# Kernel tuning notes

Hardware: AMD Instinct MI355X
Metric: run time of the kernel (lower is better)

The kernel has to match this reference:

```python
import jax, jax.numpy as jnp
import numpy as np
import math

D_MODEL = 1024
NHEAD = 16
D_HEAD = D_MODEL // NHEAD
TAU = 300.0
DELTA = 5.0 * 60.0  # delta_minutes -> seconds


def setup_inputs() -> dict:
    key = jax.random.key(0)
    ks = jax.random.split(key, 10)
    B, M = 4, 2048
    H = jax.random.normal(ks[0], (B, M, D_MODEL), dtype=jnp.float32)
    patch_mask = jax.random.randint(ks[1], (B, M), 0, 2).astype(jnp.int32)
    s = 1.0 / math.sqrt(D_MODEL)
    Wq = jax.random.normal(ks[2], (D_MODEL, D_MODEL), dtype=jnp.float32) * s
    bq = jnp.zeros((D_MODEL,), dtype=jnp.float32)
    Wk = jax.random.normal(ks[3], (D_MODEL, D_MODEL), dtype=jnp.float32) * s
    bk = jnp.zeros((D_MODEL,), dtype=jnp.float32)
    Wv = jax.random.normal(ks[4], (D_MODEL, D_MODEL), dtype=jnp.float32) * s
    bv = jnp.zeros((D_MODEL,), dtype=jnp.float32)
    Wo = jax.random.normal(ks[5], (D_MODEL, D_MODEL), dtype=jnp.float32) * s
    bo = jnp.zeros((D_MODEL,), dtype=jnp.float32)
    return {"H": H, "patch_mask": patch_mask, "Wq": Wq, "bq": bq,
            "Wk": Wk, "bk": bk, "Wv": Wv, "bv": bv, "Wo": Wo, "bo": bo}


def _time_bias(M):
    idx = jnp.arange(M)
    dist = jnp.abs(idx[:, None] - idx[None, :]).astype(jnp.float32) * DELTA
    w = jnp.exp(-dist / max(TAU, 1e-6))
    return jnp.log(w + 1e-12)  # (M, M)


def reference(H, patch_mask, Wq, bq, Wk, bk, Wv, bv, Wo, bo):
    B, M, D = H.shape
    nh, dh = NHEAD, D_HEAD
    # projections -> (B, nh, M, dh)
    q = (H @ Wq.T + bq).reshape(B, M, nh, dh).transpose(0, 2, 1, 3)
    k = (H @ Wk.T + bk).reshape(B, M, nh, dh).transpose(0, 2, 1, 3)
    v = (H @ Wv.T + bv).reshape(B, M, nh, dh).transpose(0, 2, 1, 3)
    attn = jnp.einsum('bhqd,bhkd->bhqk', q, k) / math.sqrt(dh)
    attn = attn + _time_bias(M)[None, None, :, :]
    key_pad = patch_mask <= 0  # (B, M)
    attn = jnp.where(key_pad[:, None, None, :], -1e9, attn)
    A = jax.nn.softmax(attn, axis=-1)
    out = jnp.einsum('bhqk,bhkd->bhqd', A, v)
    out = out.transpose(0, 2, 1, 3).reshape(B, M, D)
    out = out @ Wo.T + bo
    out = out * patch_mask[:, :, None].astype(out.dtype)
    return out
```

## Files before the change

### kernel.cpp

```cpp
#include <hip/hip_runtime.h>
#include <stdint.h>

typedef short short8 __attribute__((ext_vector_type(8)));
typedef float f32x4 __attribute__((ext_vector_type(4)));

#define B_    4
#define M_    2048
#define D_    1024
#define NH_   16
#define DH_   64
#define LOG2E 1.44269504f

#if __has_builtin(__builtin_amdgcn_exp2f)
#define EXP2F(x) __builtin_amdgcn_exp2f(x)
#else
#define EXP2F(x) exp2f(x)
#endif

__device__ __forceinline__ short f2bf(float f) {
  union { float f; uint32_t u; } v; v.f = f;
  uint32_t r = (v.u + 0x7fffu + ((v.u >> 16) & 1u)) >> 16;
  return (short)r;
}

__device__ __forceinline__ void gl_lds16(const void* g, void* l) {
  __builtin_amdgcn_global_load_lds(
      (__attribute__((address_space(1))) void*)(g),
      (__attribute__((address_space(3))) void*)(l),
      16, 0, 0);
}

__device__ __forceinline__ f32x4 mfma16(short8 a, short8 b, f32x4 c) {
  return __builtin_amdgcn_mfma_f32_16x16x32_bf16(a, b, c, 0, 0, 0);
}

#define VM_WAIT(N)  asm volatile("s_waitcnt vmcnt(" #N ")" ::: "memory")

__global__ __launch_bounds__(256) void cvt_all(const float* __restrict__ H,
                                               const float* __restrict__ s0,
                                               const float* __restrict__ s1,
                                               const float* __restrict__ s2,
                                               const float* __restrict__ s3,
                                               short* __restrict__ dH,
                                               short* __restrict__ d0,
                                               short* __restrict__ d1,
                                               short* __restrict__ d2,
                                               short* __restrict__ d3) {
  const int bidx = blockIdx.x;
  const float* src;
  short* dst;
  int i;
  if (bidx < 8192) {
    src = H; dst = dH; i = bidx * 256 + threadIdx.x;
  } else {
    const int y = (bidx - 8192) >> 10;
    src = (y == 0) ? s0 : (y == 1) ? s1 : (y == 2) ? s2 : s3;
    dst = (y == 0) ? d0 : (y == 1) ? d1 : (y == 2) ? d2 : d3;
    i = ((bidx - 8192) & 1023) * 256 + threadIdx.x;
  }
  float4 v = ((const float4*)src)[i];
  short4 o;
  o.x = f2bf(v.x); o.y = f2bf(v.y); o.z = f2bf(v.z); o.w = f2bf(v.w);
  ((short4*)dst)[i] = o;
}

__global__ __launch_bounds__(256, 2) void gemm_qkv(const short* __restrict__ A,
                                                   const short* __restrict__ Wqb,
                                                   const short* __restrict__ Wkb,
                                                   const short* __restrict__ Wvb,
                                                   const float* __restrict__ bq,
                                                   const float* __restrict__ bk,
                                                   const float* __restrict__ bv,
                                                   short* __restrict__ Qo,
                                                   short* __restrict__ Ko,
                                                   short* __restrict__ Vo) {
  __shared__ char smem_raw[65536];
  short* Ab0 = (short*)smem_raw;
  short* Ab1 = (short*)(smem_raw + 8192);

  const int L = blockIdx.x + 8 * blockIdx.y;
  const int xcd = L & 7;
  const int s = L >> 3;
  const int m_local = s & 7;
  const int nt = s >> 3;
  const int m0 = (xcd * 8 + m_local) * 128;
  const int n0 = nt * 128;

  const int tid = threadIdx.x;
  const int w = tid >> 6, l = tid & 63;
  const int q4 = l >> 4, c = l & 15;
  const int wr = w >> 1, wc = w & 1;

  f32x4 acc[3][4][4] = {};
  const int arow = (l >> 2);
  const int acol = ((l & 3) ^ ((l >> 3) & 3)) * 8;
  const int q4s = (q4 ^ ((c >> 1) & 3)) * 8;

  const short* Bz0 = Wqb;
  const short* Bz1 = Wkb;
  const short* Bz2 = Wvb;

#pragma unroll
  for (int st = 0; st < 2; ++st) {
    const int chunk = w * 2 + st;
    const size_t roff = (size_t)(chunk * 16 + arow) * 1024 + acol;
    gl_lds16(A + (size_t)m0 * 1024 + roff, Ab0 + chunk * 512);
    gl_lds16(Bz0 + (size_t)n0 * 1024 + roff, (short*)(smem_raw + 16384) + chunk * 512);
    gl_lds16(Bz1 + (size_t)n0 * 1024 + roff, (short*)(smem_raw + 32768) + chunk * 512);
    gl_lds16(Bz2 + (size_t)n0 * 1024 + roff, (short*)(smem_raw + 49152) + chunk * 512);
  }
  __syncthreads();

  for (int kk = 0; kk < 32; ++kk) {
    const int cur = kk & 1;
    if (kk + 1 < 32) {
      const int k0n = (kk + 1) * 32;
#pragma unroll
      for (int st = 0; st < 2; ++st) {
        const int chunk = w * 2 + st;
        const size_t roff = (size_t)(chunk * 16 + arow) * 1024 + k0n + acol;
        gl_lds16(A + (size_t)m0 * 1024 + roff, (cur ? Ab0 : Ab1) + chunk * 512);
        gl_lds16(Bz0 + (size_t)n0 * 1024 + roff,
                 (short*)(smem_raw + 16384 + (cur ? 0 : 8192)) + chunk * 512);
        gl_lds16(Bz1 + (size_t)n0 * 1024 + roff,
                 (short*)(smem_raw + 32768 + (cur ? 0 : 8192)) + chunk * 512);
        gl_lds16(Bz2 + (size_t)n0 * 1024 + roff,
                 (short*)(smem_raw + 49152 + (cur ? 0 : 8192)) + chunk * 512);
      }
    }
    const short* Ab = cur ? Ab1 : Ab0;
    short8 af[4];
#pragma unroll
    for (int i = 0; i < 4; ++i)
      af[i] = *(const short8*)(Ab + (wr * 64 + i * 16 + c) * 32 + q4s);
#pragma unroll
    for (int z = 0; z < 3; ++z) {
      const short* Bb =
          (const short*)(smem_raw + 16384 + z * 16384 + (cur ? 8192 : 0));
      short8 bfr[4];
#pragma unroll
      for (int j = 0; j < 4; ++j)
        bfr[j] = *(const short8*)(Bb + (wc * 64 + j * 16 + c) * 32 + q4s);
#pragma unroll
      for (int i = 0; i < 4; ++i)
#pragma unroll
        for (int j = 0; j < 4; ++j)
          acc[z][i][j] = mfma16(af[i], bfr[j], acc[z][i][j]);
    }
    __syncthreads();
  }

#pragma unroll
  for (int z = 0; z < 2; ++z) {
    short* Cb = (short*)smem_raw;
    const float* bias = z ? bk : bq;
    short* outp = z ? Ko : Qo;
    const float scale = z ? 1.0f : (0.125f * LOG2E);
#pragma unroll
    for (int j = 0; j < 4; ++j) {
      const float bvv = bias[n0 + wc * 64 + j * 16 + c];
#pragma unroll
      for (int i = 0; i < 4; ++i)
#pragma unroll
        for (int r = 0; r < 4; ++r)
          Cb[(wr * 64 + i * 16 + q4 * 4 + r) * 136 + wc * 64 + j * 16 + c] =
              f2bf((acc[z][i][j][r] + bvv) * scale);
    }
    __syncthreads();
#pragma unroll
    for (int p = 0; p < 8; ++p) {
      const int g = p * 256 + tid;
      const int row = g >> 4, seg = g & 15;
      *(short8*)(outp + (size_t)(m0 + row) * 1024 + n0 + seg * 8) =
          *(const short8*)(Cb + row * 136 + seg * 8);
    }
    __syncthreads();
  }
  {
    short* Cb = (short*)smem_raw;
#pragma unroll
    for (int j = 0; j < 4; ++j) {
      const float bvv = bv[n0 + wc * 64 + j * 16 + c];
#pragma unroll
      for (int i = 0; i < 4; ++i) {
        short4 pk;
        pk.x = f2bf(acc[2][i][j][0] + bvv);
        pk.y = f2bf(acc[2][i][j][1] + bvv);
        pk.z = f2bf(acc[2][i][j][2] + bvv);
        pk.w = f2bf(acc[2][i][j][3] + bvv);
        *(short4*)(Cb + (wc * 64 + j * 16 + c) * 136 + wr * 64 + i * 16 + q4 * 4) = pk;
      }
    }
    __syncthreads();
    const int bb = m0 >> 11;
    const int tokb = m0 & 2047;
#pragma unroll
    for (int p = 0; p < 8; ++p) {
      const int g = p * 256 + tid;
      const int col = g >> 4, rseg = g & 15;
      const int colg = n0 + col;
      const int hh = colg >> 6, dd = colg & 63;
      *(short8*)(Vo + ((size_t)(bb * NH_ + hh) * DH_ + dd) * M_ + tokb + rseg * 8) =
          *(const short8*)(Cb + col * 136 + rseg * 8);
    }
  }
}

__global__ __launch_bounds__(256, 2) void gemm_oproj(const short* __restrict__ A,
                                                     const short* __restrict__ Bt,
                                                     const float* __restrict__ bias,
                                                     const int* __restrict__ pmask,
                                                     float* __restrict__ outp) {
  __shared__ char smem[33792];
  short* Ab0 = (short*)smem;
  short* Ab1 = (short*)(smem + 8192);
  short* Bb0 = (short*)(smem + 16384);
  short* Bb1 = (short*)(smem + 24576);

  const int L = blockIdx.x + 8 * blockIdx.y;
  const int xcd = L & 7;
  const int s = L >> 3;
  const int m_local = s & 7;
  const int nt = s >> 3;
  const int m0 = (xcd * 8 + m_local) * 128;
  const int n0 = nt * 128;

  const int tid = threadIdx.x;
  const int w = tid >> 6, l = tid & 63;
  const int q4 = l >> 4, c = l & 15;
  const int wr = w >> 1, wc = w & 1;

  f32x4 acc[4][4] = {};
  const int arow = (l >> 2);
  const int acol = ((l & 3) ^ ((l >> 3) & 3)) * 8;
  const int q4s = (q4 ^ ((c >> 1) & 3)) * 8;

#pragma unroll
  for (int st = 0; st < 2; ++st) {
    const int chunk = w * 2 + st;
    const size_t roff = (size_t)(chunk * 16 + arow) * 1024 + acol;
    gl_lds16(A + (size_t)m0 * 1024 + roff, Ab0 + chunk * 512);
    gl_lds16(Bt + (size_t)n0 * 1024 + roff, Bb0 + chunk * 512);
  }
  __syncthreads();

  for (int kk = 0; kk < 32; ++kk) {
    const int cur = kk & 1;
    if (kk + 1 < 32) {
      const int k0n = (kk + 1) * 32;
#pragma unroll
      for (int st = 0; st < 2; ++st) {
        const int chunk = w * 2 + st;
        const size_t roff = (size_t)(chunk * 16 + arow) * 1024 + k0n + acol;
        gl_lds16(A + (size_t)m0 * 1024 + roff, (cur ? Ab0 : Ab1) + chunk * 512);
        gl_lds16(Bt + (size_t)n0 * 1024 + roff, (cur ? Bb0 : Bb1) + chunk * 512);
      }
    }
    const short* Ab = cur ? Ab1 : Ab0;
    const short* Bb = cur ? Bb1 : Bb0;
    short8 af[4], bfr[4];
#pragma unroll
    for (int i = 0; i < 4; ++i)
      af[i] = *(const short8*)(Ab + (wr * 64 + i * 16 + c) * 32 + q4s);
#pragma unroll
    for (int j = 0; j < 4; ++j)
      bfr[j] = *(const short8*)(Bb + (wc * 64 + j * 16 + c) * 32 + q4s);
#pragma unroll
    for (int i = 0; i < 4; ++i)
#pragma unroll
      for (int j = 0; j < 4; ++j)
        acc[i][j] = mfma16(af[i], bfr[j], acc[i][j]);
    __syncthreads();
  }

  float* Cf = (float*)smem;
#pragma unroll
  for (int half = 0; half < 2; ++half) {
    __syncthreads();
    if (wr == half) {
#pragma unroll
      for (int j = 0; j < 4; ++j) {
        const float bvv = bias[n0 + wc * 64 + j * 16 + c];
#pragma unroll
        for (int i = 0; i < 4; ++i)
#pragma unroll
          for (int r = 0; r < 4; ++r)
            Cf[(i * 16 + q4 * 4 + r) * 132 + wc * 64 + j * 16 + c] =
                acc[i][j][r] + bvv;
      }
    }
    __syncthreads();
#pragma unroll
    for (int p = 0; p < 8; ++p) {
      const int g = p * 256 + tid;
      const int row = g >> 5, seg = g & 31;
      const int rowg = m0 + half * 64 + row;
      const float mmv = (pmask[rowg] > 0) ? 1.0f : 0.0f;
      float4 v = *(const float4*)(Cf + row * 132 + seg * 4);
      v.x *= mmv; v.y *= mmv; v.z *= mmv; v.w *= mmv;
      *(float4*)(outp + (size_t)rowg * 1024 + n0 + seg * 4) = v;
    }
  }
}

__global__ __launch_bounds__(256) void attn_kernel(const short* __restrict__ Qb,
                                                   const short* __restrict__ Kb,
                                                   const short* __restrict__ Vtb,
                                                   const int* __restrict__ pmask,
                                                   short* __restrict__ Attb) {
  __shared__ char smem[20480];
  short* Ks0 = (short*)smem;
  short* Ks1 = (short*)(smem + 4096);
  short* Vs0 = (short*)(smem + 8192);
  short* Vs1 = (short*)(smem + 12288);
  short* Ps  = (short*)(smem + 16384);

  const int tid = threadIdx.x;
  const int w = tid >> 6, l = tid & 63;
  const int q4 = l >> 4, c = l & 15;
  const int qt = blockIdx.x, h = blockIdx.y, b = blockIdx.z;
  const short* Qrow = Qb + (size_t)(b * M_) * D_ + h * DH_;
  const short* Kbase = Kb + (size_t)(b * M_) * D_ + h * DH_;
  const short* Vbase = Vtb + (size_t)(b * NH_ + h) * DH_ * M_;
  const int* pm = pmask + b * M_;
  const int qrow0 = qt * 64 + w * 16;

  short8 aq0 = *(const short8*)(Qrow + (size_t)(qrow0 + c) * D_ + q4 * 8);
  short8 aq1 = *(const short8*)(Qrow + (size_t)(qrow0 + c) * D_ + 32 + q4 * 8);

  const int jt0 = max(0, 2 * qt - 2);
  const int jt1 = min(M_ / 32 - 1, 2 * qt + 3);

  const int kh = tid >> 7, krow = (tid >> 2) & 31, ch = tid & 3;
  const int vrow = tid >> 2;

  {
    const int j0 = jt0 * 32;
    gl_lds16(Kbase + (size_t)(j0 + krow) * D_ + kh * 32 + ch * 8, (char*)Ks0 + tid * 16);
    gl_lds16(Vbase + (size_t)vrow * M_ + j0 + ch * 8, (char*)Vs0 + tid * 16);
  }

  f32x4 o[4] = {};
  float lrun[4] = {0.f, 0.f, 0.f, 0.f};
  short* Pw = Ps + w * 512;
  const int ib = qrow0 + q4 * 4 - c;
  const float CLAMP = 28.0f * LOG2E;
  const float C16   = 16.0f * LOG2E;

  for (int jt = jt0; jt <= jt1; ++jt) {
    const int buf = (jt - jt0) & 1;
    const int j0 = jt * 32;
    if (jt < jt1) {
      const int j0n = j0 + 32;
      gl_lds16(Kbase + (size_t)(j0n + krow) * D_ + kh * 32 + ch * 8,
               (char*)(buf ? Ks0 : Ks1) + tid * 16);
      gl_lds16(Vbase + (size_t)vrow * M_ + j0n + ch * 8,
               (char*)(buf ? Vs0 : Vs1) + tid * 16);
      VM_WAIT(2);
    } else {
      VM_WAIT(0);
    }
    __builtin_amdgcn_sched_barrier(0);
    __builtin_amdgcn_s_barrier();
    __builtin_amdgcn_sched_barrier(0);

    const short* Kt = buf ? Ks1 : Ks0;
    const short* Vt = buf ? Vs1 : Vs0;
    short8 b00 = *(const short8*)(Kt + c * 32 + q4 * 8);
    short8 b10 = *(const short8*)(Kt + 1024 + c * 32 + q4 * 8);
    short8 b01 = *(const short8*)(Kt + (16 + c) * 32 + q4 * 8);
    short8 b11 = *(const short8*)(Kt + 1024 + (16 + c) * 32 + q4 * 8);
    f32x4 s0 = {}, s1 = {};
    __builtin_amdgcn_s_setprio(1);
    s0 = mfma16(aq0, b00, s0);
    s0 = mfma16(aq1, b10, s0);
    s1 = mfma16(aq0, b01, s1);
    s1 = mfma16(aq1, b11, s1);
    __builtin_amdgcn_s_setprio(0);

    const float w0m = (pm[j0 + c] > 0) ? 1.f : 0.f;
    const float w1m = (pm[j0 + 16 + c] > 0) ? 1.f : 0.f;
    const float eb = (float)(ib - j0) * LOG2E;

#pragma unroll
    for (int r = 0; r < 4; ++r) {
      const float er = eb + (float)r * LOG2E;
      const float d0 = fminf(fabsf(er), CLAMP);
      const float d1 = fminf(fabsf(er - C16), CLAMP);
      const float p0 = EXP2F(s0[r] - d0) * w0m;
      const float p1 = EXP2F(s1[r] - d1) * w1m;
      Pw[(q4 * 4 + r) * 32 + c] = f2bf(p0);
      Pw[(q4 * 4 + r) * 32 + 16 + c] = f2bf(p1);
      lrun[r] += p0 + p1;
    }
    short8 pa = *(const short8*)(Pw + c * 32 + q4 * 8);
    __builtin_amdgcn_s_setprio(1);
#pragma unroll
    for (int f = 0; f < 4; ++f) {
      short8 bv = *(const short8*)(Vt + (f * 16 + c) * 32 + q4 * 8);
      o[f] = mfma16(pa, bv, o[f]);
    }
    __builtin_amdgcn_s_setprio(0);
    __builtin_amdgcn_sched_barrier(0);
    __builtin_amdgcn_s_barrier();
  }

#pragma unroll
  for (int r = 0; r < 4; ++r) {
#pragma unroll
    for (int off = 1; off < 16; off <<= 1)
      lrun[r] += __shfl_xor(lrun[r], off);
  }

  short* Cb = (short*)smem;
#pragma unroll
  for (int r = 0; r < 4; ++r) {
    const float inv = 1.0f / lrun[r];
#pragma unroll
    for (int f = 0; f < 4; ++f)
      Cb[(w * 16 + q4 * 4 + r) * 72 + f * 16 + c] = f2bf(o[f][r] * inv);
  }
  __syncthreads();
#pragma unroll
  for (int p = 0; p < 2; ++p) {
    const int u = p * 256 + tid;
    const int row = u >> 3, seg = u & 7;
    *(short8*)(Attb + (size_t)(b * M_ + qt * 64 + row) * D_ + h * DH_ + seg * 8) =
        *(const short8*)(Cb + row * 72 + seg * 8);
  }
}

extern "C" void kernel_launch(void* const* d_in, const int* in_sizes, int n_in,
                              void* d_out, int out_size, void* d_ws, size_t ws_size,
                              hipStream_t stream) {
  const float* H     = (const float*)d_in[0];
  const int*   pmask = (const int*)d_in[1];
  const float* Wq    = (const float*)d_in[2];
  const float* bq    = (const float*)d_in[3];
  const float* Wk    = (const float*)d_in[4];
  const float* bk    = (const float*)d_in[5];
  const float* Wv    = (const float*)d_in[6];
  const float* bv    = (const float*)d_in[7];
  const float* Wo    = (const float*)d_in[8];
  const float* bo    = (const float*)d_in[9];
  float* out = (float*)d_out;
  char* ws = (char*)d_ws;

  short* Hb   = (short*)(ws);
  short* Attb = (short*)(ws);
  short* Wqb  = (short*)(ws + (16u << 20));
  short* Wkb  = (short*)(ws + (18u << 20));
  short* Wvb  = (short*)(ws + (20u << 20));
  short* Wob  = (short*)(ws + (22u << 20));
  short* Qb   = (short*)(ws + (24u << 20));
  short* Kb2  = (short*)(ws + (40u << 20));
  short* Vtb  = (short*)(ws + (56u << 20));

  cvt_all<<<8192 + 4096, 256, 0, stream>>>(H, Wq, Wk, Wv, Wo,
                                           Hb, Wqb, Wkb, Wvb, Wob);

  gemm_qkv<<<dim3(8, 64), 256, 0, stream>>>(Hb, Wqb, Wkb, Wvb, bq, bk, bv,
                                            Qb, Kb2, Vtb);

  attn_kernel<<<dim3(M_ / 64, NH_, B_), 256, 0, stream>>>(Qb, Kb2, Vtb, pmask, Attb);

  gemm_oproj<<<dim3(8, 64), 256, 0, stream>>>(Attb, Wob, bo, pmask, out);
}
```

Before: 208.6 us.

## Restructure QKV GEMM into per-projection 256x128 tiles with deeper async pipeline

The fused QKV GEMM, which computed all three projections per 128x128 block, becomes one projection per block with 256x128 tiles, 512 threads and 768 blocks. The K loop now keeps four stages of global-to-LDS loads in flight, waits on explicit vmcnt counts with raw barriers, and raises wave priority around the MFMA bursts. This is meant to hide load latency and improve occupancy and balance across CUs. The cost is 96KB of LDS per block, A-tile reloads repeated for each projection, and fragile hand-tuned wait counts.

```diff
diff --git a/kernel.cpp b/kernel.cpp
--- a/kernel.cpp
+++ b/kernel.cpp
@@ -35,6 +35,9 @@
 }
 
 #define VM_WAIT(N)  asm volatile("s_waitcnt vmcnt(" #N ")" ::: "memory")
+#define BAR_FENCE()                    \
+  __builtin_amdgcn_s_barrier();        \
+  __builtin_amdgcn_sched_barrier(0)
 
 __global__ __launch_bounds__(256) void cvt_all(const float* __restrict__ H,
                                                const float* __restrict__ s0,
@@ -64,7 +67,7 @@
   ((short4*)dst)[i] = o;
 }
 
-__global__ __launch_bounds__(256, 2) void gemm_qkv(const short* __restrict__ A,
+__global__ __launch_bounds__(512, 2) void gemm_qkv(const short* __restrict__ A,
                                                    const short* __restrict__ Wqb,
                                                    const short* __restrict__ Wkb,
                                                    const short* __restrict__ Wvb,
@@ -74,121 +77,123 @@
                                                    short* __restrict__ Qo,
                                                    short* __restrict__ Ko,
                                                    short* __restrict__ Vo) {
-  __shared__ char smem_raw[65536];
-  short* Ab0 = (short*)smem_raw;
-  short* Ab1 = (short*)(smem_raw + 8192);
-
-  const int L = blockIdx.x + 8 * blockIdx.y;
+  __shared__ char smem[98304];
+
+  const int L = blockIdx.x;
   const int xcd = L & 7;
-  const int s = L >> 3;
-  const int m_local = s & 7;
-  const int nt = s >> 3;
-  const int m0 = (xcd * 8 + m_local) * 128;
+  const int sL = L >> 3;
+  const int m_local = sL & 3;
+  const int nt = (sL >> 2) & 7;
+  const int z = sL >> 5;
+  const int m0 = (xcd * 4 + m_local) * 256;
   const int n0 = nt * 128;
+
+  const short* Bz = (z == 0) ? Wqb : (z == 1) ? Wkb : Wvb;
+  const float* bias = (z == 0) ? bq : (z == 1) ? bk : bv;
 
   const int tid = threadIdx.x;
   const int w = tid >> 6, l = tid & 63;
   const int q4 = l >> 4, c = l & 15;
   const int wr = w >> 1, wc = w & 1;
 
-  f32x4 acc[3][4][4] = {};
+  f32x4 acc[4][4] = {};
+
   const int arow = (l >> 2);
   const int acol = ((l & 3) ^ ((l >> 3) & 3)) * 8;
   const int q4s = (q4 ^ ((c >> 1) & 3)) * 8;
 
-  const short* Bz0 = Wqb;
-  const short* Bz1 = Wkb;
-  const short* Bz2 = Wvb;
-
-#pragma unroll
-  for (int st = 0; st < 2; ++st) {
-    const int chunk = w * 2 + st;
-    const size_t roff = (size_t)(chunk * 16 + arow) * 1024 + acol;
-    gl_lds16(A + (size_t)m0 * 1024 + roff, Ab0 + chunk * 512);
-    gl_lds16(Bz0 + (size_t)n0 * 1024 + roff, (short*)(smem_raw + 16384) + chunk * 512);
-    gl_lds16(Bz1 + (size_t)n0 * 1024 + roff, (short*)(smem_raw + 32768) + chunk * 512);
-    gl_lds16(Bz2 + (size_t)n0 * 1024 + roff, (short*)(smem_raw + 49152) + chunk * 512);
-  }
+  const size_t gA0 = (size_t)(m0 + w * 32 + arow) * 1024 + acol;
+  const size_t gA1 = (size_t)(m0 + w * 32 + 16 + arow) * 1024 + acol;
+  const size_t gB  = (size_t)(n0 + w * 16 + arow) * 1024 + acol;
+  const int dA0 = (w * 128 + l) * 8;
+  const int dA1 = (w * 128 + 64 + l) * 8;
+  const int dB  = (w * 64 + l) * 8;
+
+#define STAGE(I, S, H)                                                        \
+  do {                                                                        \
+    short* As_ = (short*)(smem + (I)*32768 + (S)*16384);                      \
+    short* Bs_ = (short*)(smem + 65536 + (I)*16384 + (S)*8192);               \
+    const size_t ko_ = (size_t)(H)*32;                                        \
+    gl_lds16(A + gA0 + ko_, As_ + dA0);                                       \
+    gl_lds16(A + gA1 + ko_, As_ + dA1);                                       \
+    gl_lds16(Bz + gB + ko_, Bs_ + dB);                                        \
+  } while (0)
+
+#define PHASE(I, S, WAITN)                                                    \
+  do {                                                                        \
+    VM_WAIT(WAITN);                                                           \
+    BAR_FENCE();                                                              \
+    const short* As_ = (const short*)(smem + (I)*32768 + (S)*16384);          \
+    const short* Bs_ = (const short*)(smem + 65536 + (I)*16384 + (S)*8192);   \
+    short8 af[4], bfr[4];                                                     \
+    _Pragma("unroll") for (int m = 0; m < 4; ++m)                             \
+        af[m] = *(const short8*)(As_ + (wr * 64 + m * 16 + c) * 32 + q4s);    \
+    _Pragma("unroll") for (int n = 0; n < 4; ++n)                             \
+        bfr[n] = *(const short8*)(Bs_ + (wc * 64 + n * 16 + c) * 32 + q4s);   \
+    __builtin_amdgcn_s_setprio(1);                                            \
+    _Pragma("unroll") for (int m = 0; m < 4; ++m)                             \
+        _Pragma("unroll") for (int n = 0; n < 4; ++n)                         \
+            acc[m][n] = mfma16(af[m], bfr[n], acc[m][n]);                     \
+    __builtin_amdgcn_s_setprio(0);                                            \
+    BAR_FENCE();                                                              \
+  } while (0)
+
+  STAGE(0, 0, 0);
+  STAGE(0, 1, 1);
+  STAGE(1, 0, 2);
+  STAGE(1, 1, 3);
+
+  for (int hh = 0; hh < 28; hh += 4) {
+    PHASE(0, 0, 9); STAGE(0, 0, hh + 4);
+    PHASE(0, 1, 9); STAGE(0, 1, hh + 5);
+    PHASE(1, 0, 9); STAGE(1, 0, hh + 6);
+    PHASE(1, 1, 9); STAGE(1, 1, hh + 7);
+  }
+  PHASE(0, 0, 9);
+  PHASE(0, 1, 6);
+  PHASE(1, 0, 3);
+  PHASE(1, 1, 0);
+
+#undef STAGE
+#undef PHASE
+
   __syncthreads();
 
-  for (int kk = 0; kk < 32; ++kk) {
-    const int cur = kk & 1;
-    if (kk + 1 < 32) {
-      const int k0n = (kk + 1) * 32;
-#pragma unroll
-      for (int st = 0; st < 2; ++st) {
-        const int chunk = w * 2 + st;
-        const size_t roff = (size_t)(chunk * 16 + arow) * 1024 + k0n + acol;
-        gl_lds16(A + (size_t)m0 * 1024 + roff, (cur ? Ab0 : Ab1) + chunk * 512);
-        gl_lds16(Bz0 + (size_t)n0 * 1024 + roff,
-                 (short*)(smem_raw + 16384 + (cur ? 0 : 8192)) + chunk * 512);
-        gl_lds16(Bz1 + (size_t)n0 * 1024 + roff,
-                 (short*)(smem_raw + 32768 + (cur ? 0 : 8192)) + chunk * 512);
-        gl_lds16(Bz2 + (size_t)n0 * 1024 + roff,
-                 (short*)(smem_raw + 49152 + (cur ? 0 : 8192)) + chunk * 512);
-      }
-    }
-    const short* Ab = cur ? Ab1 : Ab0;
-    short8 af[4];
-#pragma unroll
-    for (int i = 0; i < 4; ++i)
-      af[i] = *(const short8*)(Ab + (wr * 64 + i * 16 + c) * 32 + q4s);
-#pragma unroll
-    for (int z = 0; z < 3; ++z) {
-      const short* Bb =
-          (const short*)(smem_raw + 16384 + z * 16384 + (cur ? 8192 : 0));
-      short8 bfr[4];
-#pragma unroll
-      for (int j = 0; j < 4; ++j)
-        bfr[j] = *(const short8*)(Bb + (wc * 64 + j * 16 + c) * 32 + q4s);
-#pragma unroll
-      for (int i = 0; i < 4; ++i)
-#pragma unroll
-        for (int j = 0; j < 4; ++j)
-          acc[z][i][j] = mfma16(af[i], bfr[j], acc[z][i][j]);
-    }
-    __syncthreads();
-  }
-
-#pragma unroll
-  for (int z = 0; z < 2; ++z) {
-    short* Cb = (short*)smem_raw;
-    const float* bias = z ? bk : bq;
+  if (z < 2) {
+    short* Cb = (short*)smem;
     short* outp = z ? Ko : Qo;
     const float scale = z ? 1.0f : (0.125f * LOG2E);
 #pragma unroll
-    for (int j = 0; j < 4; ++j) {
-      const float bvv = bias[n0 + wc * 64 + j * 16 + c];
-#pragma unroll
-      for (int i = 0; i < 4; ++i)
+    for (int n = 0; n < 4; ++n) {
+      const float bvv = bias[n0 + wc * 64 + n * 16 + c];
+#pragma unroll
+      for (int m = 0; m < 4; ++m)
 #pragma unroll
         for (int r = 0; r < 4; ++r)
-          Cb[(wr * 64 + i * 16 + q4 * 4 + r) * 136 + wc * 64 + j * 16 + c] =
-              f2bf((acc[z][i][j][r] + bvv) * scale);
+          Cb[(wr * 64 + m * 16 + q4 * 4 + r) * 136 + wc * 64 + n * 16 + c] =
+              f2bf((acc[m][n][r] + bvv) * scale);
     }
     __syncthreads();
 #pragma unroll
     for (int p = 0; p < 8; ++p) {
-      const int g = p * 256 + tid;
+      const int g = p * 512 + tid;
       const int row = g >> 4, seg = g & 15;
       *(short8*)(outp + (size_t)(m0 + row) * 1024 + n0 + seg * 8) =
           *(const short8*)(Cb + row * 136 + seg * 8);
     }
-    __syncthreads();
-  }
-  {
-    short* Cb = (short*)smem_raw;
-#pragma unroll
-    for (int j = 0; j < 4; ++j) {
-      const float bvv = bv[n0 + wc * 64 + j * 16 + c];
-#pragma unroll
-      for (int i = 0; i < 4; ++i) {
+  } else {
+    short* Cb = (short*)smem;
+#pragma unroll
+    for (int n = 0; n < 4; ++n) {
+      const float bvv = bias[n0 + wc * 64 + n * 16 + c];
+#pragma unroll
+      for (int m = 0; m < 4; ++m) {
         short4 pk;
-        pk.x = f2bf(acc[2][i][j][0] + bvv);
-        pk.y = f2bf(acc[2][i][j][1] + bvv);
-        pk.z = f2bf(acc[2][i][j][2] + bvv);
-        pk.w = f2bf(acc[2][i][j][3] + bvv);
-        *(short4*)(Cb + (wc * 64 + j * 16 + c) * 136 + wr * 64 + i * 16 + q4 * 4) = pk;
+        pk.x = f2bf(acc[m][n][0] + bvv);
+        pk.y = f2bf(acc[m][n][1] + bvv);
+        pk.z = f2bf(acc[m][n][2] + bvv);
+        pk.w = f2bf(acc[m][n][3] + bvv);
+        *(short4*)(Cb + (wc * 64 + n * 16 + c) * 264 + wr * 64 + m * 16 + q4 * 4) = pk;
       }
     }
     __syncthreads();
@@ -196,12 +201,12 @@
     const int tokb = m0 & 2047;
 #pragma unroll
     for (int p = 0; p < 8; ++p) {
-      const int g = p * 256 + tid;
-      const int col = g >> 4, rseg = g & 15;
+      const int g = p * 512 + tid;
+      const int col = g >> 5, rseg = g & 31;
       const int colg = n0 + col;
-      const int hh = colg >> 6, dd = colg & 63;
-      *(short8*)(Vo + ((size_t)(bb * NH_ + hh) * DH_ + dd) * M_ + tokb + rseg * 8) =
-          *(const short8*)(Cb + col * 136 + rseg * 8);
+      const int hh2 = colg >> 6, dd = colg & 63;
+      *(short8*)(Vo + ((size_t)(bb * NH_ + hh2) * DH_ + dd) * M_ + tokb + rseg * 8) =
+          *(const short8*)(Cb + col * 264 + rseg * 8);
     }
   }
 }
@@ -459,8 +464,8 @@
   cvt_all<<<8192 + 4096, 256, 0, stream>>>(H, Wq, Wk, Wv, Wo,
                                            Hb, Wqb, Wkb, Wvb, Wob);
 
-  gemm_qkv<<<dim3(8, 64), 256, 0, stream>>>(Hb, Wqb, Wkb, Wvb, bq, bk, bv,
-                                            Qb, Kb2, Vtb);
+  gemm_qkv<<<768, 512, 0, stream>>>(Hb, Wqb, Wkb, Wvb, bq, bk, bv,
+                                    Qb, Kb2, Vtb);
 
   attn_kernel<<<dim3(M_ / 64, NH_, B_), 256, 0, stream>>>(Qb, Kb2, Vtb, pmask, Attb);
 
```

Result: slower. 225.0 us (+7.9%).
